# Optimization experiments

Hardware: AMD Instinct MI355X
Metric: run time of the kernel (lower is better)

The kernel has to match this reference:

```python
import jax, jax.numpy as jnp
import numpy as np

B = 64          # graphs per batch
MAX_NODES = 512 # nodes per graph
N = B * MAX_NODES
DEG = 16
E = N * DEG
F_IN = 12
H, D = 4, 32    # heads, per-head dim
HID = H * D     # 128
A = 512         # num_outputs (action space)
NEG_SLOPE = 0.2


def setup_inputs() -> dict:
    key = jax.random.key(0)
    ks = jax.random.split(key, 32)
    x = jax.random.normal(ks[0], (N, F_IN), dtype=jnp.float32)
    # edges confined within each graph's node block (as in the torch adjacency loop)
    src_l = jax.random.randint(ks[1], (B, MAX_NODES * DEG), 0, MAX_NODES, dtype=jnp.int32)
    dst_l = jax.random.randint(ks[2], (B, MAX_NODES * DEG), 0, MAX_NODES, dtype=jnp.int32)
    offs = (jnp.arange(B, dtype=jnp.int32) * MAX_NODES)[:, None]
    edge_src = (src_l + offs).reshape(-1)
    edge_dst = (dst_l + offs).reshape(-1)
    batch_idx = jnp.repeat(jnp.arange(B, dtype=jnp.int32), MAX_NODES)

    s = 0.1
    p = {}
    p["Wl0"] = s * jax.random.normal(ks[3], (F_IN, H, D), dtype=jnp.float32)
    p["Wr0"] = s * jax.random.normal(ks[4], (F_IN, H, D), dtype=jnp.float32)
    p["att0"] = s * jax.random.normal(ks[5], (H, D), dtype=jnp.float32)
    p["b0"] = jnp.zeros((HID,), dtype=jnp.float32)
    p["Wl"] = s * jax.random.normal(ks[6], (3, HID, H, D), dtype=jnp.float32)
    p["Wr"] = s * jax.random.normal(ks[7], (3, HID, H, D), dtype=jnp.float32)
    p["att"] = s * jax.random.normal(ks[8], (3, H, D), dtype=jnp.float32)
    p["b"] = jnp.zeros((3, HID), dtype=jnp.float32)
    p["qW1"] = s * jax.random.normal(ks[9], (2 * HID, HID), dtype=jnp.float32)
    p["qb1"] = jnp.zeros((HID,), dtype=jnp.float32)
    p["qW2"] = s * jax.random.normal(ks[10], (HID, A), dtype=jnp.float32)
    p["qb2"] = jnp.zeros((A,), dtype=jnp.float32)
    p["vW1"] = s * jax.random.normal(ks[11], (2 * HID, HID), dtype=jnp.float32)
    p["vb1"] = jnp.zeros((HID,), dtype=jnp.float32)
    p["vW2"] = s * jax.random.normal(ks[12], (HID, 1), dtype=jnp.float32)
    p["vb2"] = jnp.zeros((1,), dtype=jnp.float32)
    return dict(x=x, edge_src=edge_src, edge_dst=edge_dst, batch_idx=batch_idx, **p)


def _gatv2(x, src, dst, Wl, Wr, att, b):
    n = x.shape[0]
    xl = jnp.einsum('nf,fhd->nhd', x, Wl)  # source transform [N,H,D]
    xr = jnp.einsum('nf,fhd->nhd', x, Wr)  # target transform [N,H,D]
    xj = xl[src]                            # [E,H,D]
    e = jax.nn.leaky_relu(xj + xr[dst], NEG_SLOPE)
    s = jnp.einsum('ehd,hd->eh', e, att)    # [E,H]
    smax = jax.ops.segment_max(s, dst, num_segments=n)
    smax = jnp.where(jnp.isfinite(smax), smax, 0.0)
    a = jnp.exp(s - smax[dst])
    den = jax.ops.segment_sum(a, dst, num_segments=n)
    a = a / jnp.maximum(den[dst], 1e-16)
    out = jax.ops.segment_sum(a[:, :, None] * xj, dst, num_segments=n)  # [N,H,D]
    return out.reshape(n, H * D) + b


def reference(x, edge_src, edge_dst, batch_idx,
              Wl0, Wr0, att0, b0, Wl, Wr, att, b,
              qW1, qb1, qW2, qb2, vW1, vb1, vW2, vb2):
    h = jax.nn.relu(_gatv2(x, edge_src, edge_dst, Wl0, Wr0, att0, b0))
    for i in range(3):  # remaining num_layers-1 GATv2 layers (dropout off in eval)
        h = jax.nn.relu(_gatv2(h, edge_src, edge_dst, Wl[i], Wr[i], att[i], b[i]))
    nb = h.shape[0] // MAX_NODES
    gsum = jax.ops.segment_sum(h, batch_idx, num_segments=nb)
    cnt = jax.ops.segment_sum(jnp.ones((h.shape[0], 1), h.dtype), batch_idx, num_segments=nb)
    gmean = gsum / jnp.maximum(cnt, 1.0)
    gmax = jax.ops.segment_max(h, batch_idx, num_segments=nb)
    g = jnp.concatenate([gmean, gmax], axis=-1)  # [B, 2*HID]
    adv = jax.nn.relu(g @ qW1 + qb1) @ qW2 + qb2
    val = jax.nn.relu(g @ vW1 + vb1) @ vW2 + vb2
    q = val + (adv - adv.mean(axis=-1, keepdims=True))
    return q
```

## Files before the change

kernel.cpp:

```cpp
#include <hip/hip_runtime.h>
#include <hip/hip_bf16.h>

#define NN 32768
#define EE 524288
#define HID 128
#define BGRAPH 64
#define MAXN 512
#define AOUT 512
#define MAXDEG 64

typedef __attribute__((ext_vector_type(8))) short short8;
typedef __attribute__((ext_vector_type(4))) float f32x4;
typedef unsigned short ushort;
typedef unsigned int uint;

__device__ __forceinline__ ushort bf16_rn(float f) {
    uint u = __float_as_uint(f);
    u += 0x7FFF + ((u >> 16) & 1);
    return (ushort)(u >> 16);
}
__device__ __forceinline__ void bf16_split(float f, ushort& hi, ushort& lo) {
    hi = bf16_rn(f);
    float fh = __uint_as_float(((uint)hi) << 16);
    lo = bf16_rn(f - fh);
}

__global__ __launch_bounds__(256) void setup_kernel(
    const int* __restrict__ src, const int* __restrict__ dst,
    int* __restrict__ cursor, int* __restrict__ bucket,
    const float* __restrict__ Wl, const float* __restrict__ Wr,
    ushort* __restrict__ wt_hi, ushort* __restrict__ wt_lo) {
    int blk = blockIdx.x;
    if (blk < EE / 256) {
        int i = blk * 256 + threadIdx.x;
        int d = dst[i];
        int p = atomicAdd(&cursor[d], 1);
        if (p < MAXDEG) bucket[(size_t)d * MAXDEG + p] = src[i];
    } else {
        int idx = (blk - EE / 256) * 256 + threadIdx.x;
        if (idx >= 98304) return;
        int c = idx & 127;
        int k = (idx >> 7) & 127;
        int l = (idx >> 14) % 3;
        int lr = idx / 49152;
        float v = (lr ? Wr : Wl)[l * 16384 + k * 128 + c];
        ushort hi, lo;
        bf16_split(v, hi, lo);
        int ct = c >> 4, m = c & 15;
        int ks = k >> 5;
        int lane = (((k >> 3) & 3) << 4) | m;
        int j = k & 7;
        size_t o = ((size_t)(lr * 3 + l) * 32 + ct * 4 + ks) * 512 + lane * 8 + j;
        wt_hi[o] = hi;
        wt_lo[o] = lo;
    }
}

template<int KTOT, int KC>
__global__ __launch_bounds__(256) void transform3(
    const float* __restrict__ hin, const float* __restrict__ Wl,
    const float* __restrict__ Wr, float* __restrict__ xl, float* __restrict__ xr) {
    __shared__ float wb[KC][256];
    __shared__ float ha[KC][36];
    int b = blockIdx.x;
    int xcd = b & 7, slot = b >> 3;
    int graph = xcd + 8 * (slot >> 4);
    int chunk = slot & 15;
    int node0 = graph * 512 + chunk * 32;
    int t = threadIdx.x;
    int c32 = t & 31;
    int ng  = t >> 5;
    const float4* wl4g = (const float4*)Wl;
    const float4* wr4g = (const float4*)Wr;
    for (int idx = t; idx < KC * 64; idx += 256) {
        int k = idx >> 6, r = idx & 63;
        float4 v = (r < 32) ? wl4g[k * 32 + r] : wr4g[k * 32 + (r - 32)];
        ((float4*)&wb[k][0])[r] = v;
    }
    for (int idx = t; idx < 32 * KC; idx += 256) {
        int m = idx / KC, kk = idx - m * KC;
        ha[kk][m] = hin[(size_t)(node0 + m) * KTOT + kk];
    }
    __syncthreads();
    float4 accL[4], accR[4];
#pragma unroll
    for (int m = 0; m < 4; m++) {
        accL[m].x = accL[m].y = accL[m].z = accL[m].w = 0.f;
        accR[m].x = accR[m].y = accR[m].z = accR[m].w = 0.f;
    }
#pragma unroll
    for (int kk = 0; kk < KC; kk++) {
        float4 wl = ((const float4*)&wb[kk][0])[c32];
        float4 wr = ((const float4*)&wb[kk][128])[c32];
        float4 hv = *(const float4*)&ha[kk][ng * 4];
        accL[0].x = fmaf(hv.x, wl.x, accL[0].x); accL[0].y = fmaf(hv.x, wl.y, accL[0].y);
        accL[0].z = fmaf(hv.x, wl.z, accL[0].z); accL[0].w = fmaf(hv.x, wl.w, accL[0].w);
        accL[1].x = fmaf(hv.y, wl.x, accL[1].x); accL[1].y = fmaf(hv.y, wl.y, accL[1].y);
        accL[1].z = fmaf(hv.y, wl.z, accL[1].z); accL[1].w = fmaf(hv.y, wl.w, accL[1].w);
        accL[2].x = fmaf(hv.z, wl.x, accL[2].x); accL[2].y = fmaf(hv.z, wl.y, accL[2].y);
        accL[2].z = fmaf(hv.z, wl.z, accL[2].z); accL[2].w = fmaf(hv.z, wl.w, accL[2].w);
        accL[3].x = fmaf(hv.w, wl.x, accL[3].x); accL[3].y = fmaf(hv.w, wl.y, accL[3].y);
        accL[3].z = fmaf(hv.w, wl.z, accL[3].z); accL[3].w = fmaf(hv.w, wl.w, accL[3].w);
        accR[0].x = fmaf(hv.x, wr.x, accR[0].x); accR[0].y = fmaf(hv.x, wr.y, accR[0].y);
        accR[0].z = fmaf(hv.x, wr.z, accR[0].z); accR[0].w = fmaf(hv.x, wr.w, accR[0].w);
        accR[1].x = fmaf(hv.y, wr.x, accR[1].x); accR[1].y = fmaf(hv.y, wr.y, accR[1].y);
        accR[1].z = fmaf(hv.y, wr.z, accR[1].z); accR[1].w = fmaf(hv.y, wr.w, accR[1].w);
        accR[2].x = fmaf(hv.z, wr.x, accR[2].x); accR[2].y = fmaf(hv.z, wr.y, accR[2].y);
        accR[2].z = fmaf(hv.z, wr.z, accR[2].z); accR[2].w = fmaf(hv.z, wr.w, accR[2].w);
        accR[3].x = fmaf(hv.w, wr.x, accR[3].x); accR[3].y = fmaf(hv.w, wr.y, accR[3].y);
        accR[3].z = fmaf(hv.w, wr.z, accR[3].z); accR[3].w = fmaf(hv.w, wr.w, accR[3].w);
    }
    float4* xlo = (float4*)xl;
    float4* xro = (float4*)xr;
#pragma unroll
    for (int m = 0; m < 4; m++) {
        int n = node0 + ng * 4 + m;
        xlo[n * 32 + c32] = accL[m];
        xro[n * 32 + c32] = accR[m];
    }
}

__global__ __launch_bounds__(256) void transform_mfma(
    const ushort* __restrict__ hhi, const ushort* __restrict__ hlo,
    const ushort* __restrict__ wl_hi, const ushort* __restrict__ wl_lo,
    const ushort* __restrict__ wr_hi, const ushort* __restrict__ wr_lo,
    float* __restrict__ xl, float* __restrict__ xr) {
    int b = blockIdx.x;
    int xcd = b & 7, slot = b >> 3;
    int graph = xcd + 8 * (slot >> 3);
    int chunk = slot & 7;
    int node0 = graph * 512 + chunk * 64 + (threadIdx.x >> 6) * 16;
    int lane = threadIdx.x & 63;
    int m = lane & 15, quad = lane >> 4;
    int tg = node0 >> 4;

    f32x4 accL[8], accR[8];
#pragma unroll
    for (int ct = 0; ct < 8; ct++) {
        accL[ct] = (f32x4){0.f, 0.f, 0.f, 0.f};
        accR[ct] = (f32x4){0.f, 0.f, 0.f, 0.f};
    }
#pragma unroll
    for (int ks = 0; ks < 4; ks++) {
        size_t ab = ((size_t)(tg * 4 + ks) * 64 + lane) * 8;
        short8 ah = *(const short8*)(hhi + ab);
        short8 al = *(const short8*)(hlo + ab);
#pragma unroll
        for (int ct = 0; ct < 8; ct++) {
            size_t wb = ((size_t)(ct * 4 + ks) * 64 + lane) * 8;
            short8 bhl = *(const short8*)(wl_hi + wb);
            short8 bll = *(const short8*)(wl_lo + wb);
            short8 bhr = *(const short8*)(wr_hi + wb);
            short8 blr = *(const short8*)(wr_lo + wb);
            accL[ct] = __builtin_amdgcn_mfma_f32_16x16x32_bf16(ah, bhl, accL[ct], 0, 0, 0);
            accL[ct] = __builtin_amdgcn_mfma_f32_16x16x32_bf16(ah, bll, accL[ct], 0, 0, 0);
            accL[ct] = __builtin_amdgcn_mfma_f32_16x16x32_bf16(al, bhl, accL[ct], 0, 0, 0);
            accR[ct] = __builtin_amdgcn_mfma_f32_16x16x32_bf16(ah, bhr, accR[ct], 0, 0, 0);
            accR[ct] = __builtin_amdgcn_mfma_f32_16x16x32_bf16(ah, blr, accR[ct], 0, 0, 0);
            accR[ct] = __builtin_amdgcn_mfma_f32_16x16x32_bf16(al, bhr, accR[ct], 0, 0, 0);
        }
    }
#pragma unroll
    for (int ct = 0; ct < 8; ct++) {
#pragma unroll
        for (int r = 0; r < 4; r++) {
            int node = node0 + quad * 4 + r;
            xl[(size_t)node * 128 + ct * 16 + m] = accL[ct][r];
            xr[(size_t)node * 128 + ct * 16 + m] = accR[ct][r];
        }
    }
}

__device__ __forceinline__ void gat_node2(
    const float4* __restrict__ xl4, const float4* __restrict__ xr4,
    const int* __restrict__ brow, int nE, int n, int el2, int p16,
    const float4& at0, const float4& at1, float4& o0, float4& o1) {
    float4 xr0 = xr4[(size_t)n * 32 + p16 * 2];
    float4 xr1 = xr4[(size_t)n * 32 + p16 * 2 + 1];
    float4 acc0, acc1;
    acc0.x = acc0.y = acc0.z = acc0.w = 0.f;
    acc1.x = acc1.y = acc1.z = acc1.w = 0.f;
    float den = 0.f;
    int nB = (nE + 7) >> 3;
    for (int blk = 0; blk < nB; blk++) {
        int ebase = blk * 8 + el2 * 4;
        int4 i4 = *(const int4*)(brow + ebase);
#pragma unroll
        for (int c = 0; c < 4; c++) {
            int e = ebase + c;
            int raw = (c == 0) ? i4.x : (c == 1) ? i4.y : (c == 2) ? i4.z : i4.w;
            int s = (e < nE) ? raw : n;
            const float4* row = xl4 + (size_t)s * 32 + p16 * 2;
            float4 v0 = row[0];
            float4 v1 = row[1];
            float t = 0.f, u, lr;
            u = v0.x + xr0.x; lr = fmaf(0.2f, fminf(u, 0.f), fmaxf(u, 0.f)); t = fmaf(at0.x, lr, t);
            u = v0.y + xr0.y; lr = fmaf(0.2f, fminf(u, 0.f), fmaxf(u, 0.f)); t = fmaf(at0.y, lr, t);
            u = v0.z + xr0.z; lr = fmaf(0.2f, fminf(u, 0.f), fmaxf(u, 0.f)); t = fmaf(at0.z, lr, t);
            u = v0.w + xr0.w; lr = fmaf(0.2f, fminf(u, 0.f), fmaxf(u, 0.f)); t = fmaf(at0.w, lr, t);
            u = v1.x + xr1.x; lr = fmaf(0.2f, fminf(u, 0.f), fmaxf(u, 0.f)); t = fmaf(at1.x, lr, t);
            u = v1.y + xr1.y; lr = fmaf(0.2f, fminf(u, 0.f), fmaxf(u, 0.f)); t = fmaf(at1.y, lr, t);
            u = v1.z + xr1.z; lr = fmaf(0.2f, fminf(u, 0.f), fmaxf(u, 0.f)); t = fmaf(at1.z, lr, t);
            u = v1.w + xr1.w; lr = fmaf(0.2f, fminf(u, 0.f), fmaxf(u, 0.f)); t = fmaf(at1.w, lr, t);
            t += __shfl_xor(t, 1);
            t += __shfl_xor(t, 2);
            float a = (e < nE) ? __expf(t) : 0.f;
            den += a;
            acc0.x = fmaf(a, v0.x, acc0.x); acc0.y = fmaf(a, v0.y, acc0.y);
            acc0.z = fmaf(a, v0.z, acc0.z); acc0.w = fmaf(a, v0.w, acc0.w);
            acc1.x = fmaf(a, v1.x, acc1.x); acc1.y = fmaf(a, v1.y, acc1.y);
            acc1.z = fmaf(a, v1.z, acc1.z); acc1.w = fmaf(a, v1.w, acc1.w);
        }
    }
    acc0.x += __shfl_xor(acc0.x, 16); acc0.y += __shfl_xor(acc0.y, 16);
    acc0.z += __shfl_xor(acc0.z, 16); acc0.w += __shfl_xor(acc0.w, 16);
    acc1.x += __shfl_xor(acc1.x, 16); acc1.y += __shfl_xor(acc1.y, 16);
    acc1.z += __shfl_xor(acc1.z, 16); acc1.w += __shfl_xor(acc1.w, 16);
    den += __shfl_xor(den, 16);
    float rden = 1.0f / fmaxf(den, 1e-16f);
    o0.x = acc0.x * rden; o0.y = acc0.y * rden;
    o0.z = acc0.z * rden; o0.w = acc0.w * rden;
    o1.x = acc1.x * rden; o1.y = acc1.y * rden;
    o1.z = acc1.z * rden; o1.w = acc1.w * rden;
}

__global__ __launch_bounds__(256) void gat_aggregate_h(
    const float* __restrict__ xl, const float* __restrict__ xr,
    const int* __restrict__ bucket, const int* __restrict__ cnt,
    const float* __restrict__ att, const float* __restrict__ bias,
    ushort* __restrict__ hhi, ushort* __restrict__ hlo) {
    int b = blockIdx.x;
    int xcd = b & 7, slot = b >> 3;
    int graph = xcd + 8 * (slot >> 5);
    int chunk = slot & 31;
    int wid = threadIdx.x >> 6;
    int lane = threadIdx.x & 63;
    int n0 = graph * 512 + chunk * 16 + wid * 4;
    int nh  = lane >> 5;
    int el2 = (lane >> 4) & 1;
    int p16 = lane & 15;
    const float4* xl4 = (const float4*)xl;
    const float4* xr4 = (const float4*)xr;
    const float4* att4 = (const float4*)att;
    float4 at0 = att4[p16 * 2];
    float4 at1 = att4[p16 * 2 + 1];
#pragma unroll 1
    for (int ni = 0; ni < 2; ni++) {
        int n = n0 + ni * 2 + nh;
        int nE = cnt[n];
        nE = (nE > MAXDEG) ? MAXDEG : nE;
        float4 o0, o1;
        gat_node2(xl4, xr4, bucket + (size_t)n * MAXDEG, nE, n, el2, p16,
                  at0, at1, o0, o1);
        if (el2 == 0) {
            const float4* bias4 = (const float4*)bias;
            float4 b0v = bias4[p16 * 2];
            float4 b1v = bias4[p16 * 2 + 1];
            float f[8];
            f[0] = fmaxf(o0.x + b0v.x, 0.f); f[1] = fmaxf(o0.y + b0v.y, 0.f);
            f[2] = fmaxf(o0.z + b0v.z, 0.f); f[3] = fmaxf(o0.w + b0v.w, 0.f);
            f[4] = fmaxf(o1.x + b1v.x, 0.f); f[5] = fmaxf(o1.y + b1v.y, 0.f);
            f[6] = fmaxf(o1.z + b1v.z, 0.f); f[7] = fmaxf(o1.w + b1v.w, 0.f);
            ushort hi[8], lo[8];
#pragma unroll
            for (int i = 0; i < 8; i++) bf16_split(f[i], hi[i], lo[i]);
            uint4 ph, pl;
            ph.x = (uint)hi[0] | ((uint)hi[1] << 16);
            ph.y = (uint)hi[2] | ((uint)hi[3] << 16);
            ph.z = (uint)hi[4] | ((uint)hi[5] << 16);
            ph.w = (uint)hi[6] | ((uint)hi[7] << 16);
            pl.x = (uint)lo[0] | ((uint)lo[1] << 16);
            pl.y = (uint)lo[2] | ((uint)lo[3] << 16);
            pl.z = (uint)lo[4] | ((uint)lo[5] << 16);
            pl.w = (uint)lo[6] | ((uint)lo[7] << 16);
            size_t base = (((size_t)(n >> 4) * 4 + (p16 >> 2)) * 64
                           + (p16 & 3) * 16 + (n & 15)) * 8;
            *(uint4*)(hhi + base) = ph;
            *(uint4*)(hlo + base) = pl;
        }
    }
}

__global__ __launch_bounds__(256) void agg_pool(
    const float* __restrict__ xl_in, const float* __restrict__ xr_in,
    const int* __restrict__ bucket, const int* __restrict__ cnt,
    const float* __restrict__ att, const float* __restrict__ bias,
    float* __restrict__ psum, float* __restrict__ pmax) {
    __shared__ float sums[4][128];
    __shared__ float maxs[4][128];
    int b = blockIdx.x;
    int xcd = b & 7, slot = b >> 3;
    int graph = xcd + 8 * (slot >> 5);
    int chunk = slot & 31;
    int wid = threadIdx.x >> 6;
    int lane = threadIdx.x & 63;
    int n0 = graph * 512 + chunk * 16 + wid * 4;
    int nh  = lane >> 5;
    int el2 = (lane >> 4) & 1;
    int p16 = lane & 15;
    const float4* xl4 = (const float4*)xl_in;
    const float4* xr4 = (const float4*)xr_in;
    const float4* att4 = (const float4*)att;
    const float4* bias4 = (const float4*)bias;
    float4 at0 = att4[p16 * 2];
    float4 at1 = att4[p16 * 2 + 1];
    float4 b0v = bias4[p16 * 2];
    float4 b1v = bias4[p16 * 2 + 1];
    float4 s0, s1, m0, m1;
    s0.x = s0.y = s0.z = s0.w = 0.f;
    s1.x = s1.y = s1.z = s1.w = 0.f;
    m0.x = m0.y = m0.z = m0.w = -1e30f;
    m1.x = m1.y = m1.z = m1.w = -1e30f;
#pragma unroll 1
    for (int ni = 0; ni < 2; ni++) {
        int n = n0 + ni * 2 + nh;
        int nE = cnt[n];
        nE = (nE > MAXDEG) ? MAXDEG : nE;
        float4 o0, o1;
        gat_node2(xl4, xr4, bucket + (size_t)n * MAXDEG, nE, n, el2, p16,
                  at0, at1, o0, o1);
        o0.x = fmaxf(o0.x + b0v.x, 0.f); o0.y = fmaxf(o0.y + b0v.y, 0.f);
        o0.z = fmaxf(o0.z + b0v.z, 0.f); o0.w = fmaxf(o0.w + b0v.w, 0.f);
        o1.x = fmaxf(o1.x + b1v.x, 0.f); o1.y = fmaxf(o1.y + b1v.y, 0.f);
        o1.z = fmaxf(o1.z + b1v.z, 0.f); o1.w = fmaxf(o1.w + b1v.w, 0.f);
        s0.x += o0.x; s0.y += o0.y; s0.z += o0.z; s0.w += o0.w;
        s1.x += o1.x; s1.y += o1.y; s1.z += o1.z; s1.w += o1.w;
        m0.x = fmaxf(m0.x, o0.x); m0.y = fmaxf(m0.y, o0.y);
        m0.z = fmaxf(m0.z, o0.z); m0.w = fmaxf(m0.w, o0.w);
        m1.x = fmaxf(m1.x, o1.x); m1.y = fmaxf(m1.y, o1.y);
        m1.z = fmaxf(m1.z, o1.z); m1.w = fmaxf(m1.w, o1.w);
    }
    s0.x += __shfl_xor(s0.x, 32); s0.y += __shfl_xor(s0.y, 32);
    s0.z += __shfl_xor(s0.z, 32); s0.w += __shfl_xor(s0.w, 32);
    s1.x += __shfl_xor(s1.x, 32); s1.y += __shfl_xor(s1.y, 32);
    s1.z += __shfl_xor(s1.z, 32); s1.w += __shfl_xor(s1.w, 32);
    m0.x = fmaxf(m0.x, __shfl_xor(m0.x, 32)); m0.y = fmaxf(m0.y, __shfl_xor(m0.y, 32));
    m0.z = fmaxf(m0.z, __shfl_xor(m0.z, 32)); m0.w = fmaxf(m0.w, __shfl_xor(m0.w, 32));
    m1.x = fmaxf(m1.x, __shfl_xor(m1.x, 32)); m1.y = fmaxf(m1.y, __shfl_xor(m1.y, 32));
    m1.z = fmaxf(m1.z, __shfl_xor(m1.z, 32)); m1.w = fmaxf(m1.w, __shfl_xor(m1.w, 32));
    if (nh == 0 && el2 == 0) {
        *(float4*)&sums[wid][p16 * 8]     = s0;
        *(float4*)&sums[wid][p16 * 8 + 4] = s1;
        *(float4*)&maxs[wid][p16 * 8]     = m0;
        *(float4*)&maxs[wid][p16 * 8 + 4] = m1;
    }
    __syncthreads();
    int t = threadIdx.x;
    if (t < 128) {
        float s = 0.f, m = -1e30f;
#pragma unroll
        for (int ww = 0; ww < 4; ww++) {
            s += sums[ww][t];
            m = fmaxf(m, maxs[ww][t]);
        }
        psum[((size_t)graph * 32 + chunk) * 128 + t] = s;
        pmax[((size_t)graph * 32 + chunk) * 128 + t] = m;
    }
}

__global__ __launch_bounds__(512) void head_kernel(
    const float* __restrict__ psum, const float* __restrict__ pmax,
    const float* __restrict__ qW1, const float* __restrict__ qb1,
    const float* __restrict__ qW2, const float* __restrict__ qb2,
    const float* __restrict__ vW1, const float* __restrict__ vb1,
    const float* __restrict__ vW2, const float* __restrict__ vb2,
    float* __restrict__ qout) {
    __shared__ float gs[256];
    __shared__ float hq[128];
    __shared__ float hv[128];
    __shared__ float red[512];
    int b = blockIdx.x, t = threadIdx.x;
    if (t < 128) {
        float s = 0.f, m = -1e30f;
#pragma unroll 8
        for (int c = 0; c < 32; c++) {
            s += psum[((size_t)b * 32 + c) * 128 + t];
            m = fmaxf(m, pmax[((size_t)b * 32 + c) * 128 + t]);
        }
        gs[t] = s * (1.0f / 512.0f);
        gs[128 + t] = m;
    }
    __syncthreads();
    if (t < 128) {
        float acc = qb1[t];
        for (int k = 0; k < 256; k++) acc = fmaf(gs[k], qW1[k * 128 + t], acc);
        hq[t] = fmaxf(acc, 0.f);
    } else if (t < 256) {
        int tt = t - 128;
        float acc = vb1[tt];
        for (int k = 0; k < 256; k++) acc = fmaf(gs[k], vW1[k * 128 + tt], acc);
        hv[tt] = fmaxf(acc, 0.f);
    }
    __syncthreads();
    float adv = qb2[t];
    for (int k = 0; k < 128; k++) adv = fmaf(hq[k], qW2[k * 512 + t], adv);
    red[t] = (t < 128) ? hv[t] * vW2[t] : 0.f;
    __syncthreads();
    for (int off = 256; off > 0; off >>= 1) {
        if (t < off) red[t] += red[t + off];
        __syncthreads();
    }
    float val = red[0] + vb2[0];
    __syncthreads();
    red[t] = adv;
    __syncthreads();
    for (int off = 256; off > 0; off >>= 1) {
        if (t < off) red[t] += red[t + off];
        __syncthreads();
    }
    float mean_adv = red[0] * (1.0f / 512.0f);
    qout[b * 512 + t] = val + adv - mean_adv;
}

extern "C" void kernel_launch(void* const* d_in, const int* in_sizes, int n_in,
                              void* d_out, int out_size, void* d_ws, size_t ws_size,
                              hipStream_t stream) {
    const float* x        = (const float*)d_in[0];
    const int* edge_src   = (const int*)d_in[1];
    const int* edge_dst   = (const int*)d_in[2];
    const float* Wl0 = (const float*)d_in[4];
    const float* Wr0 = (const float*)d_in[5];
    const float* att0 = (const float*)d_in[6];
    const float* b0 = (const float*)d_in[7];
    const float* Wl = (const float*)d_in[8];
    const float* Wr = (const float*)d_in[9];
    const float* att = (const float*)d_in[10];
    const float* bb = (const float*)d_in[11];
    const float* qW1 = (const float*)d_in[12];
    const float* qb1 = (const float*)d_in[13];
    const float* qW2 = (const float*)d_in[14];
    const float* qb2 = (const float*)d_in[15];
    const float* vW1 = (const float*)d_in[16];
    const float* vb1 = (const float*)d_in[17];
    const float* vW2 = (const float*)d_in[18];
    const float* vb2 = (const float*)d_in[19];

    int* cursor  = (int*)d_ws;
    int* bucket  = cursor + NN;
    float* fbase = (float*)(bucket + (size_t)NN * MAXDEG);
    float* xl    = fbase;
    float* xr    = xl + NN * 128;
    float* psum  = xr + NN * 128;
    float* pmax  = psum + BGRAPH * 32 * 128;
    ushort* hhi  = (ushort*)(pmax + BGRAPH * 32 * 128);
    ushort* hlo  = hhi + (size_t)NN * 128;
    ushort* wthi = hlo + (size_t)NN * 128;
    ushort* wtlo = wthi + 2 * 3 * 16384;

    hipMemsetAsync(cursor, 0, NN * sizeof(int), stream);
    setup_kernel<<<EE / 256 + 384, 256, 0, stream>>>(edge_src, edge_dst, cursor, bucket,
                                                     Wl, Wr, wthi, wtlo);

    transform3<12, 12><<<NN / 32, 256, 0, stream>>>(x, Wl0, Wr0, xl, xr);
    gat_aggregate_h<<<NN / 16, 256, 0, stream>>>(xl, xr, bucket, cursor, att0, b0, hhi, hlo);

    for (int i = 0; i < 3; i++) {
        const ushort* wl_hi = wthi + (size_t)i * 16384;
        const ushort* wl_lo = wtlo + (size_t)i * 16384;
        const ushort* wr_hi = wthi + (size_t)(3 + i) * 16384;
        const ushort* wr_lo = wtlo + (size_t)(3 + i) * 16384;
        transform_mfma<<<NN / 64, 256, 0, stream>>>(hhi, hlo, wl_hi, wl_lo, wr_hi, wr_lo,
                                                    xl, xr);
        if (i < 2) {
            gat_aggregate_h<<<NN / 16, 256, 0, stream>>>(xl, xr, bucket, cursor,
                                                         att + i * 128, bb + i * 128,
                                                         hhi, hlo);
        } else {
            agg_pool<<<NN / 16, 256, 0, stream>>>(xl, xr, bucket, cursor,
                                                  att + 256, bb + 256, psum, pmax);
        }
    }
    head_kernel<<<BGRAPH, 512, 0, stream>>>(psum, pmax, qW1, qb1, qW2, qb2,
                                            vW1, vb1, vW2, vb2, (float*)d_out);
}
```

Baseline: 310.3 us.

## Fuse GAT aggregation with next layer's MFMA transform via shared memory

Merges the aggregation kernel and the following bf16-split MFMA linear transform into one kernel. The aggregated 16-node tile is staged in LDS instead of being written to global hhi/hlo and read back, and each wave computes two column tiles of the next layer's xl/xr. Because other blocks still read the previous layer's features while this one writes, xl/xr are ping-ponged between two buffer sets. This removes three kernel launches and the global round trip of the intermediate h, but weights are now reloaded per 16-node block rather than per 64-node block, and a block barrier is added.

```diff
diff --git a/kernel.cpp b/kernel.cpp
--- a/kernel.cpp
+++ b/kernel.cpp
@@ -120,57 +120,6 @@
     }
 }
 
-__global__ __launch_bounds__(256) void transform_mfma(
-    const ushort* __restrict__ hhi, const ushort* __restrict__ hlo,
-    const ushort* __restrict__ wl_hi, const ushort* __restrict__ wl_lo,
-    const ushort* __restrict__ wr_hi, const ushort* __restrict__ wr_lo,
-    float* __restrict__ xl, float* __restrict__ xr) {
-    int b = blockIdx.x;
-    int xcd = b & 7, slot = b >> 3;
-    int graph = xcd + 8 * (slot >> 3);
-    int chunk = slot & 7;
-    int node0 = graph * 512 + chunk * 64 + (threadIdx.x >> 6) * 16;
-    int lane = threadIdx.x & 63;
-    int m = lane & 15, quad = lane >> 4;
-    int tg = node0 >> 4;
-
-    f32x4 accL[8], accR[8];
-#pragma unroll
-    for (int ct = 0; ct < 8; ct++) {
-        accL[ct] = (f32x4){0.f, 0.f, 0.f, 0.f};
-        accR[ct] = (f32x4){0.f, 0.f, 0.f, 0.f};
-    }
-#pragma unroll
-    for (int ks = 0; ks < 4; ks++) {
-        size_t ab = ((size_t)(tg * 4 + ks) * 64 + lane) * 8;
-        short8 ah = *(const short8*)(hhi + ab);
-        short8 al = *(const short8*)(hlo + ab);
-#pragma unroll
-        for (int ct = 0; ct < 8; ct++) {
-            size_t wb = ((size_t)(ct * 4 + ks) * 64 + lane) * 8;
-            short8 bhl = *(const short8*)(wl_hi + wb);
-            short8 bll = *(const short8*)(wl_lo + wb);
-            short8 bhr = *(const short8*)(wr_hi + wb);
-            short8 blr = *(const short8*)(wr_lo + wb);
-            accL[ct] = __builtin_amdgcn_mfma_f32_16x16x32_bf16(ah, bhl, accL[ct], 0, 0, 0);
-            accL[ct] = __builtin_amdgcn_mfma_f32_16x16x32_bf16(ah, bll, accL[ct], 0, 0, 0);
-            accL[ct] = __builtin_amdgcn_mfma_f32_16x16x32_bf16(al, bhl, accL[ct], 0, 0, 0);
-            accR[ct] = __builtin_amdgcn_mfma_f32_16x16x32_bf16(ah, bhr, accR[ct], 0, 0, 0);
-            accR[ct] = __builtin_amdgcn_mfma_f32_16x16x32_bf16(ah, blr, accR[ct], 0, 0, 0);
-            accR[ct] = __builtin_amdgcn_mfma_f32_16x16x32_bf16(al, bhr, accR[ct], 0, 0, 0);
-        }
-    }
-#pragma unroll
-    for (int ct = 0; ct < 8; ct++) {
-#pragma unroll
-        for (int r = 0; r < 4; r++) {
-            int node = node0 + quad * 4 + r;
-            xl[(size_t)node * 128 + ct * 16 + m] = accL[ct][r];
-            xr[(size_t)node * 128 + ct * 16 + m] = accR[ct][r];
-        }
-    }
-}
-
 __device__ __forceinline__ void gat_node2(
     const float4* __restrict__ xl4, const float4* __restrict__ xr4,
     const int* __restrict__ brow, int nE, int n, int el2, int p16,
@@ -224,59 +173,103 @@
     o1.z = acc1.z * rden; o1.w = acc1.w * rden;
 }
 
-__global__ __launch_bounds__(256) void gat_aggregate_h(
-    const float* __restrict__ xl, const float* __restrict__ xr,
+__global__ __launch_bounds__(256) void fused_agg_mfma(
+    const float* __restrict__ xl_in, const float* __restrict__ xr_in,
     const int* __restrict__ bucket, const int* __restrict__ cnt,
     const float* __restrict__ att, const float* __restrict__ bias,
-    ushort* __restrict__ hhi, ushort* __restrict__ hlo) {
+    const ushort* __restrict__ wl_hi, const ushort* __restrict__ wl_lo,
+    const ushort* __restrict__ wr_hi, const ushort* __restrict__ wr_lo,
+    float* __restrict__ xl_out, float* __restrict__ xr_out) {
+    __shared__ ushort hh[16][136];
+    __shared__ ushort hl[16][136];
     int b = blockIdx.x;
     int xcd = b & 7, slot = b >> 3;
     int graph = xcd + 8 * (slot >> 5);
     int chunk = slot & 31;
+    int node_base = graph * 512 + chunk * 16;
     int wid = threadIdx.x >> 6;
     int lane = threadIdx.x & 63;
-    int n0 = graph * 512 + chunk * 16 + wid * 4;
+    int n0 = node_base + wid * 4;
     int nh  = lane >> 5;
     int el2 = (lane >> 4) & 1;
     int p16 = lane & 15;
-    const float4* xl4 = (const float4*)xl;
-    const float4* xr4 = (const float4*)xr;
-    const float4* att4 = (const float4*)att;
-    float4 at0 = att4[p16 * 2];
-    float4 at1 = att4[p16 * 2 + 1];
+    {
+        const float4* xl4 = (const float4*)xl_in;
+        const float4* xr4 = (const float4*)xr_in;
+        const float4* att4 = (const float4*)att;
+        float4 at0 = att4[p16 * 2];
+        float4 at1 = att4[p16 * 2 + 1];
 #pragma unroll 1
-    for (int ni = 0; ni < 2; ni++) {
-        int n = n0 + ni * 2 + nh;
-        int nE = cnt[n];
-        nE = (nE > MAXDEG) ? MAXDEG : nE;
-        float4 o0, o1;
-        gat_node2(xl4, xr4, bucket + (size_t)n * MAXDEG, nE, n, el2, p16,
-                  at0, at1, o0, o1);
-        if (el2 == 0) {
-            const float4* bias4 = (const float4*)bias;
-            float4 b0v = bias4[p16 * 2];
-            float4 b1v = bias4[p16 * 2 + 1];
-            float f[8];
-            f[0] = fmaxf(o0.x + b0v.x, 0.f); f[1] = fmaxf(o0.y + b0v.y, 0.f);
-            f[2] = fmaxf(o0.z + b0v.z, 0.f); f[3] = fmaxf(o0.w + b0v.w, 0.f);
-            f[4] = fmaxf(o1.x + b1v.x, 0.f); f[5] = fmaxf(o1.y + b1v.y, 0.f);
-            f[6] = fmaxf(o1.z + b1v.z, 0.f); f[7] = fmaxf(o1.w + b1v.w, 0.f);
-            ushort hi[8], lo[8];
-#pragma unroll
-            for (int i = 0; i < 8; i++) bf16_split(f[i], hi[i], lo[i]);
-            uint4 ph, pl;
-            ph.x = (uint)hi[0] | ((uint)hi[1] << 16);
-            ph.y = (uint)hi[2] | ((uint)hi[3] << 16);
-            ph.z = (uint)hi[4] | ((uint)hi[5] << 16);
-            ph.w = (uint)hi[6] | ((uint)hi[7] << 16);
-            pl.x = (uint)lo[0] | ((uint)lo[1] << 16);
-            pl.y = (uint)lo[2] | ((uint)lo[3] << 16);
-            pl.z = (uint)lo[4] | ((uint)lo[5] << 16);
-            pl.w = (uint)lo[6] | ((uint)lo[7] << 16);
-            size_t base = (((size_t)(n >> 4) * 4 + (p16 >> 2)) * 64
-                           + (p16 & 3) * 16 + (n & 15)) * 8;
-            *(uint4*)(hhi + base) = ph;
-            *(uint4*)(hlo + base) = pl;
+        for (int ni = 0; ni < 2; ni++) {
+            int n = n0 + ni * 2 + nh;
+            int nE = cnt[n];
+            nE = (nE > MAXDEG) ? MAXDEG : nE;
+            float4 o0, o1;
+            gat_node2(xl4, xr4, bucket + (size_t)n * MAXDEG, nE, n, el2, p16,
+                      at0, at1, o0, o1);
+            if (el2 == 0) {
+                const float4* bias4 = (const float4*)bias;
+                float4 b0v = bias4[p16 * 2];
+                float4 b1v = bias4[p16 * 2 + 1];
+                float f[8];
+                f[0] = fmaxf(o0.x + b0v.x, 0.f); f[1] = fmaxf(o0.y + b0v.y, 0.f);
+                f[2] = fmaxf(o0.z + b0v.z, 0.f); f[3] = fmaxf(o0.w + b0v.w, 0.f);
+                f[4] = fmaxf(o1.x + b1v.x, 0.f); f[5] = fmaxf(o1.y + b1v.y, 0.f);
+                f[6] = fmaxf(o1.z + b1v.z, 0.f); f[7] = fmaxf(o1.w + b1v.w, 0.f);
+                ushort hi[8], lo[8];
+#pragma unroll
+                for (int i = 0; i < 8; i++) bf16_split(f[i], hi[i], lo[i]);
+                uint4 ph, pl;
+                ph.x = (uint)hi[0] | ((uint)hi[1] << 16);
+                ph.y = (uint)hi[2] | ((uint)hi[3] << 16);
+                ph.z = (uint)hi[4] | ((uint)hi[5] << 16);
+                ph.w = (uint)hi[6] | ((uint)hi[7] << 16);
+                pl.x = (uint)lo[0] | ((uint)lo[1] << 16);
+                pl.y = (uint)lo[2] | ((uint)lo[3] << 16);
+                pl.z = (uint)lo[4] | ((uint)lo[5] << 16);
+                pl.w = (uint)lo[6] | ((uint)lo[7] << 16);
+                int nl = wid * 4 + ni * 2 + nh;
+                *(uint4*)&hh[nl][p16 * 8] = ph;
+                *(uint4*)&hl[nl][p16 * 8] = pl;
+            }
+        }
+    }
+    __syncthreads();
+    int m = lane & 15, quad = lane >> 4;
+    f32x4 accL[2], accR[2];
+#pragma unroll
+    for (int c2 = 0; c2 < 2; c2++) {
+        accL[c2] = (f32x4){0.f, 0.f, 0.f, 0.f};
+        accR[c2] = (f32x4){0.f, 0.f, 0.f, 0.f};
+    }
+#pragma unroll
+    for (int ks = 0; ks < 4; ks++) {
+        short8 ah = *(const short8*)&hh[m][ks * 32 + quad * 8];
+        short8 al = *(const short8*)&hl[m][ks * 32 + quad * 8];
+#pragma unroll
+        for (int c2 = 0; c2 < 2; c2++) {
+            int ct = wid * 2 + c2;
+            size_t wb = ((size_t)(ct * 4 + ks) * 64 + lane) * 8;
+            short8 bhl = *(const short8*)(wl_hi + wb);
+            short8 bll = *(const short8*)(wl_lo + wb);
+            short8 bhr = *(const short8*)(wr_hi + wb);
+            short8 blr = *(const short8*)(wr_lo + wb);
+            accL[c2] = __builtin_amdgcn_mfma_f32_16x16x32_bf16(ah, bhl, accL[c2], 0, 0, 0);
+            accL[c2] = __builtin_amdgcn_mfma_f32_16x16x32_bf16(ah, bll, accL[c2], 0, 0, 0);
+            accL[c2] = __builtin_amdgcn_mfma_f32_16x16x32_bf16(al, bhl, accL[c2], 0, 0, 0);
+            accR[c2] = __builtin_amdgcn_mfma_f32_16x16x32_bf16(ah, bhr, accR[c2], 0, 0, 0);
+            accR[c2] = __builtin_amdgcn_mfma_f32_16x16x32_bf16(ah, blr, accR[c2], 0, 0, 0);
+            accR[c2] = __builtin_amdgcn_mfma_f32_16x16x32_bf16(al, bhr, accR[c2], 0, 0, 0);
+        }
+    }
+#pragma unroll
+    for (int c2 = 0; c2 < 2; c2++) {
+        int ct = wid * 2 + c2;
+#pragma unroll
+        for (int r = 0; r < 4; r++) {
+            int node = node_base + quad * 4 + r;
+            xl_out[(size_t)node * 128 + ct * 16 + m] = accL[c2][r];
+            xr_out[(size_t)node * 128 + ct * 16 + m] = accR[c2][r];
         }
     }
 }
@@ -438,38 +431,36 @@
     int* cursor  = (int*)d_ws;
     int* bucket  = cursor + NN;
     float* fbase = (float*)(bucket + (size_t)NN * MAXDEG);
-    float* xl    = fbase;
-    float* xr    = xl + NN * 128;
-    float* psum  = xr + NN * 128;
+    float* xlA   = fbase;
+    float* xrA   = xlA + NN * 128;
+    float* xlB   = xrA + NN * 128;
+    float* xrB   = xlB + NN * 128;
+    float* psum  = xrB + NN * 128;
     float* pmax  = psum + BGRAPH * 32 * 128;
-    ushort* hhi  = (ushort*)(pmax + BGRAPH * 32 * 128);
-    ushort* hlo  = hhi + (size_t)NN * 128;
-    ushort* wthi = hlo + (size_t)NN * 128;
+    ushort* wthi = (ushort*)(pmax + BGRAPH * 32 * 128);
     ushort* wtlo = wthi + 2 * 3 * 16384;
 
     hipMemsetAsync(cursor, 0, NN * sizeof(int), stream);
     setup_kernel<<<EE / 256 + 384, 256, 0, stream>>>(edge_src, edge_dst, cursor, bucket,
                                                      Wl, Wr, wthi, wtlo);
 
-    transform3<12, 12><<<NN / 32, 256, 0, stream>>>(x, Wl0, Wr0, xl, xr);
-    gat_aggregate_h<<<NN / 16, 256, 0, stream>>>(xl, xr, bucket, cursor, att0, b0, hhi, hlo);
-
-    for (int i = 0; i < 3; i++) {
-        const ushort* wl_hi = wthi + (size_t)i * 16384;
-        const ushort* wl_lo = wtlo + (size_t)i * 16384;
-        const ushort* wr_hi = wthi + (size_t)(3 + i) * 16384;
-        const ushort* wr_lo = wtlo + (size_t)(3 + i) * 16384;
-        transform_mfma<<<NN / 64, 256, 0, stream>>>(hhi, hlo, wl_hi, wl_lo, wr_hi, wr_lo,
-                                                    xl, xr);
-        if (i < 2) {
-            gat_aggregate_h<<<NN / 16, 256, 0, stream>>>(xl, xr, bucket, cursor,
-                                                         att + i * 128, bb + i * 128,
-                                                         hhi, hlo);
-        } else {
-            agg_pool<<<NN / 16, 256, 0, stream>>>(xl, xr, bucket, cursor,
-                                                  att + 256, bb + 256, psum, pmax);
-        }
-    }
+    transform3<12, 12><<<NN / 32, 256, 0, stream>>>(x, Wl0, Wr0, xlA, xrA);
+
+    fused_agg_mfma<<<NN / 16, 256, 0, stream>>>(xlA, xrA, bucket, cursor, att0, b0,
+                                                wthi + 0 * 16384, wtlo + 0 * 16384,
+                                                wthi + 3 * 16384, wtlo + 3 * 16384,
+                                                xlB, xrB);
+    fused_agg_mfma<<<NN / 16, 256, 0, stream>>>(xlB, xrB, bucket, cursor, att, bb,
+                                                wthi + 1 * 16384, wtlo + 1 * 16384,
+                                                wthi + 4 * 16384, wtlo + 4 * 16384,
+                                                xlA, xrA);
+    fused_agg_mfma<<<NN / 16, 256, 0, stream>>>(xlA, xrA, bucket, cursor,
+                                                att + 128, bb + 128,
+                                                wthi + 2 * 16384, wtlo + 2 * 16384,
+                                                wthi + 5 * 16384, wtlo + 5 * 16384,
+                                                xlB, xrB);
+    agg_pool<<<NN / 16, 256, 0, stream>>>(xlB, xrB, bucket, cursor,
+                                          att + 256, bb + 256, psum, pmax);
     head_kernel<<<BGRAPH, 512, 0, stream>>>(psum, pmax, qW1, qb1, qW2, qb2,
                                             vW1, vb1, vW2, vb2, (float*)d_out);
 }
```

Measured after the change: 286.2 us. -7.8%, faster.
